# Optimization experiments

Measured on AMD Instinct MI355X. Metric: run time of the kernel, lower is better.

The kernel has to match this reference:

```python
import jax, jax.numpy as jnp
import numpy as np

K = 7          # kernel_size
PAD = 3        # padding
GROUPS = 8
OUTC = 128
INC = 128
REFINE = True


def conv1x1(x, w):
    # x: [B,C,H,W], w: [O,C] (1x1 conv, no bias)
    return jnp.einsum('oc,bchw->bohw', w, x)


def unfold2d(x, k):
    # x: [B,C,Hp,Wp] -> [B,C,h,w,k,k], stride 1 (matches torch unfold(2,k).unfold(3,k))
    B, C, Hp, Wp = x.shape
    h, w = Hp - k + 1, Wp - k + 1
    patches = jnp.stack([x[:, :, i:i + h, j:j + w] for i in range(k) for j in range(k)], axis=-1)
    return patches.reshape(B, C, h, w, k, k)


def unfold1d(x, k, axis):
    # sliding window of size k, stride 1, along axis 2 (rows) or 3 (cols)
    if axis == 2:
        h = x.shape[2] - k + 1
        return jnp.stack([x[:, :, i:i + h, :] for i in range(k)], axis=-1)  # [B,C,h,W,k]
    else:
        w = x.shape[3] - k + 1
        return jnp.stack([x[:, :, :, j:j + w] for j in range(k)], axis=-1)  # [B,C,H,w,k]


def _forward(feature_map, wq, wk, wv, rel_h, rel_w):
    c = feature_map.shape[1] // 2
    fm_t0, fm_t1 = feature_map[:, :c], feature_map[:, c:]
    B, _, H, W = fm_t0.shape
    cg = OUTC // GROUPS

    padded_t0 = jnp.pad(fm_t0, ((0, 0), (0, 0), (PAD, PAD), (PAD, PAD)))
    q = conv1x1(fm_t1, wq)                 # [B,OUTC,H,W]
    k_full = conv1x1(padded_t0, wk)        # [B,OUTC,H+2p,W+2p]
    v_full = conv1x1(padded_t0, wv)

    k_win = unfold2d(k_full, K)            # [B,OUTC,H,W,K,K]
    k_h, k_w = k_win[:, :OUTC // 2], k_win[:, OUTC // 2:]
    k_win = jnp.concatenate([k_h + rel_h, k_w + rel_w], axis=1)
    k_win = k_win.reshape(B, GROUPS, cg, H, W, K * K)
    v_win = unfold2d(v_full, K).reshape(B, GROUPS, cg, H, W, K * K)

    qg = q.reshape(B, GROUPS, cg, H, W, 1)
    attn = jax.nn.softmax(jnp.sum(qg * k_win, axis=2), axis=-1)  # [B,G,H,W,K*K]
    out = jnp.einsum('bnhwk,bnchwk->bnchw', attn, v_win).reshape(B, OUTC, H, W)

    if REFINE:
        win = 2 * K + 1
        p_col = jnp.pad(fm_t0, ((0, 0), (0, 0), (K, K), (0, 0)))
        p_row = jnp.pad(fm_t0, ((0, 0), (0, 0), (0, 0), (K, K)))
        k_col = unfold1d(conv1x1(p_col, wk), win, 2).reshape(B, GROUPS, cg, H, W, win)
        k_row = unfold1d(conv1x1(p_row, wk), win, 3).reshape(B, GROUPS, cg, H, W, win)
        v_col = unfold1d(conv1x1(p_col, wv), win, 2).reshape(B, GROUPS, cg, H, W, win)
        v_row = unfold1d(conv1x1(p_row, wv), win, 3).reshape(B, GROUPS, cg, H, W, win)

        a_row = jax.nn.softmax(jnp.sum(qg * k_row, axis=2), axis=-1)
        a_col = jax.nn.softmax(jnp.sum(qg * k_col, axis=2), axis=-1)
        out = out + jnp.einsum('bnhwk,bnchwk->bnchw', a_row, v_row).reshape(B, OUTC, H, W)
        out = out + jnp.einsum('bnhwk,bnchwk->bnchw', a_col, v_col).reshape(B, OUTC, H, W)
    return out


def setup_inputs() -> dict:
    key = jax.random.key(0)
    ks = jax.random.split(key, 6)
    B, H, W = 2, 64, 64
    feature_map = jax.random.normal(ks[0], (B, 2 * INC, H, W), dtype=jnp.float32)
    # kaiming_normal fan_out for 1x1 conv: std = sqrt(2 / outc)
    std = float(np.sqrt(2.0 / OUTC))
    wq = jax.random.normal(ks[1], (OUTC, INC), dtype=jnp.float32) * std
    wk = jax.random.normal(ks[2], (OUTC, INC), dtype=jnp.float32) * std
    wv = jax.random.normal(ks[3], (OUTC, INC), dtype=jnp.float32) * std
    rel_h = jax.random.normal(ks[4], (OUTC // 2, 1, 1, K, 1), dtype=jnp.float32)
    rel_w = jax.random.normal(ks[5], (OUTC // 2, 1, 1, 1, K), dtype=jnp.float32)
    return {"feature_map": feature_map, "wq": wq, "wk": wk, "wv": wv,
            "rel_h": rel_h, "rel_w": rel_w}


def reference(feature_map, wq, wk, wv, rel_h, rel_w):
    return _forward(feature_map, wq, wk, wv, rel_h, rel_w)
```

## Files before the change

kernel.cpp:

```cpp
#include <hip/hip_runtime.h>
#include <hip/hip_bf16.h>

__device__ __forceinline__ float bf2f(unsigned short u) {
    union { unsigned int i; float f; } v; v.i = ((unsigned int)u) << 16; return v.f;
}
__device__ __forceinline__ unsigned short f2bf(float f) {
    __hip_bfloat16 h = __float2bfloat16(f);
    return *reinterpret_cast<unsigned short*>(&h);
}


#define CANVAS_SLAB 102400

__global__ __launch_bounds__(256) void pad_zero_kernel(uint4* __restrict__ p)
{
    const size_t i = (size_t)blockIdx.x * 256 + threadIdx.x;
    p[i] = make_uint4(0u, 0u, 0u, 0u);
}

__global__ __launch_bounds__(256) void conv_kernel(
    const float* __restrict__ fm,
    const float* __restrict__ wq, const float* __restrict__ wk,
    const float* __restrict__ wv,
    float* __restrict__ Qout,
    unsigned short* __restrict__ K0,
    unsigned short* __restrict__ V0)
{
    const int sel = blockIdx.z;
    const int by  = blockIdx.y;
    const float* W = (sel == 0) ? wq : ((sel == 1) ? wk : wv);
    const int c0 = (sel == 0) ? 128 : 0;

    __shared__ float w_s[64 * 68];
    __shared__ float x_s[64 * 68];

    const int tid = threadIdx.x;
    const int P0  = blockIdx.x * 64;
    const int b   = P0 >> 12;
    const int hw0 = P0 & 4095;

    float acc[4][4];
    #pragma unroll
    for (int i = 0; i < 4; ++i)
        #pragma unroll
        for (int j = 0; j < 4; ++j) acc[i][j] = 0.f;

    const int ocb = (tid >> 4) * 4;
    const int pxb = (tid & 15) * 4;

    for (int kh = 0; kh < 128; kh += 64) {
        {
            const int o    = tid >> 2;
            const int koff = (tid & 3) * 16;
            #pragma unroll
            for (int i = 0; i < 4; ++i) {
                float4 v = *(const float4*)(W + (size_t)(by * 64 + o) * 128 + kh + koff + i * 4);
                w_s[(koff + i * 4 + 0) * 68 + o] = v.x;
                w_s[(koff + i * 4 + 1) * 68 + o] = v.y;
                w_s[(koff + i * 4 + 2) * 68 + o] = v.z;
                w_s[(koff + i * 4 + 3) * 68 + o] = v.w;
            }
        }
        {
            const int c  = tid >> 2;
            const int pc = (tid & 3) * 16;
            const float* src = fm + (((size_t)(b * 256 + c0 + kh + c)) << 12) + hw0 + pc;
            #pragma unroll
            for (int i = 0; i < 4; ++i)
                *(float4*)(&x_s[c * 68 + pc + i * 4]) = *(const float4*)(src + i * 4);
        }
        __syncthreads();
        #pragma unroll 8
        for (int k = 0; k < 64; ++k) {
            float4 wa = *(const float4*)(&w_s[k * 68 + ocb]);
            float4 xv = *(const float4*)(&x_s[k * 68 + pxb]);
            const float wf[4] = {wa.x, wa.y, wa.z, wa.w};
            const float xf[4] = {xv.x, xv.y, xv.z, xv.w};
            #pragma unroll
            for (int i = 0; i < 4; ++i)
                #pragma unroll
                for (int j = 0; j < 4; ++j) acc[i][j] += wf[i] * xf[j];
        }
        __syncthreads();
    }

    const int oc  = by * 64 + ocb;
    const int g   = oc >> 4;
    const int lci = oc & 15;
    const int hh  = hw0 >> 6;
    #pragma unroll
    for (int pj = 0; pj < 4; ++pj) {
        const int ww = pxb + pj;
        if (sel == 0) {
            const size_t base = ((((size_t)(b * 8 + g)) << 12) + (hh * 64 + ww)) * 16 + lci;
            *(float4*)(Qout + base) = make_float4(acc[0][pj], acc[1][pj], acc[2][pj], acc[3][pj]);
        } else {
            const size_t cbase = (size_t)(b * 8 + g) * CANVAS_SLAB
                               + ((size_t)((hh + 8) * 80 + (ww + 8))) * 16 + lci;
            unsigned short tmp[4];
            #pragma unroll
            for (int i = 0; i < 4; ++i) tmp[i] = f2bf(acc[i][pj]);
            unsigned short* dst = ((sel == 1) ? K0 : V0) + cbase;
            *(uint2*)dst = *(const uint2*)tmp;
        }
    }
}

struct KV16 { uint4 a, b; };
__device__ __forceinline__ KV16 ld16(const unsigned short* p) {
    KV16 r; r.a = *(const uint4*)p; r.b = *(const uint4*)(p + 8); return r;
}
__device__ __forceinline__ float dotq(const float* q, const KV16& k) {
    const unsigned short* u = (const unsigned short*)&k;
    float s = 0.f;
    #pragma unroll
    for (int c = 0; c < 16; ++c) s += q[c] * bf2f(u[c]);
    return s;
}
__device__ __forceinline__ void axpyq(float* acc, float wgt, const KV16& v) {
    const unsigned short* u = (const unsigned short*)&v;
    #pragma unroll
    for (int c = 0; c < 16; ++c) acc[c] += wgt * bf2f(u[c]);
}

__global__ __launch_bounds__(256) void attn_kernel(
    const float* __restrict__ Q,
    const unsigned short* __restrict__ K0,
    const unsigned short* __restrict__ V0,
    const float* __restrict__ rel_h,
    const float* __restrict__ rel_w,
    float* __restrict__ out)
{
    const int tid  = threadIdx.x;
    const int w    = tid & 63;
    const int h    = blockIdx.x * 4 + (tid >> 6);
    const int g    = blockIdx.y;
    const int b    = blockIdx.z / 3;
    const int part = blockIdx.z % 3;

    const size_t slabQ = ((size_t)(b * 8 + g)) << 16;
    const float* qptr = Q + slabQ + (size_t)(h * 64 + w) * 16;

    float qr[16];
    #pragma unroll
    for (int ci = 0; ci < 16; ++ci) qr[ci] = qptr[ci];

    const unsigned short* Kp = K0 + (size_t)(b * 8 + g) * CANVAS_SLAB;
    const unsigned short* Vp = V0 + (size_t)(b * 8 + g) * CANVAS_SLAB;

    #define CIDX(y, x) (((size_t)(((y) + 8) * 80 + ((x) + 8))) << 4)

    float acc[16];
    #pragma unroll
    for (int ci = 0; ci < 16; ++ci) acc[ci] = 0.f;

    if (part == 0) {
        float qrel[7];
        const float* rel = (g < 4) ? (rel_h + g * 112) : (rel_w + (g - 4) * 112);
        #pragma unroll
        for (int t = 0; t < 7; ++t) {
            float s = 0.f;
            #pragma unroll
            for (int ci = 0; ci < 16; ++ci) s += qr[ci] * rel[ci * 7 + t];
            qrel[t] = s;
        }
        const bool bias_i = (g < 4);
        float sc[49];
        float mx = -3.4e38f;
        #pragma unroll
        for (int i = 0; i < 7; ++i) {
            const int y = h + i - 3;
            #pragma unroll
            for (int j = 0; j < 7; ++j) {
                const int x = w + j - 3;
                float d = dotq(qr, ld16(Kp + CIDX(y, x)));
                d += bias_i ? qrel[i] : qrel[j];
                sc[i * 7 + j] = d;
                mx = fmaxf(mx, d);
            }
        }
        float den = 0.f;
        #pragma unroll
        for (int k = 0; k < 49; ++k) { sc[k] = __expf(sc[k] - mx); den += sc[k]; }
        const float inv = 1.f / den;
        #pragma unroll
        for (int i = 0; i < 7; ++i) {
            const int y = h + i - 3;
            #pragma unroll
            for (int j = 0; j < 7; ++j) {
                const int x = w + j - 3;
                axpyq(acc, sc[i * 7 + j] * inv, ld16(Vp + CIDX(y, x)));
            }
        }
    } else if (part == 1) {
        float sc[15];
        float mx = -3.4e38f;
        #pragma unroll
        for (int j = 0; j < 15; ++j) {
            const int x = w + j - 7;
            const float d = dotq(qr, ld16(Kp + CIDX(h, x)));
            sc[j] = d; mx = fmaxf(mx, d);
        }
        float den = 0.f;
        #pragma unroll
        for (int j = 0; j < 15; ++j) { sc[j] = __expf(sc[j] - mx); den += sc[j]; }
        const float inv = 1.f / den;
        #pragma unroll
        for (int j = 0; j < 15; ++j) {
            const int x = w + j - 7;
            axpyq(acc, sc[j] * inv, ld16(Vp + CIDX(h, x)));
        }
    } else {
        float sc[15];
        float mx = -3.4e38f;
        #pragma unroll
        for (int i = 0; i < 15; ++i) {
            const int y = h + i - 7;
            const float d = dotq(qr, ld16(Kp + CIDX(y, w)));
            sc[i] = d; mx = fmaxf(mx, d);
        }
        float den = 0.f;
        #pragma unroll
        for (int i = 0; i < 15; ++i) { sc[i] = __expf(sc[i] - mx); den += sc[i]; }
        const float inv = 1.f / den;
        #pragma unroll
        for (int i = 0; i < 15; ++i) {
            const int y = h + i - 7;
            axpyq(acc, sc[i] * inv, ld16(Vp + CIDX(y, w)));
        }
    }
    #undef CIDX

    float* op = out + (((size_t)(b * 128 + g * 16)) << 12) + h * 64 + w;
    #pragma unroll
    for (int ci = 0; ci < 16; ++ci)
        atomicAdd(op + ((size_t)ci << 12), acc[ci]);
}

extern "C" void kernel_launch(void* const* d_in, const int* in_sizes, int n_in,
                              void* d_out, int out_size, void* d_ws, size_t ws_size,
                              hipStream_t stream) {
    (void)in_sizes; (void)n_in; (void)ws_size;
    const float* fm    = (const float*)d_in[0];
    const float* wq    = (const float*)d_in[1];
    const float* wk    = (const float*)d_in[2];
    const float* wv    = (const float*)d_in[3];
    const float* rel_h = (const float*)d_in[4];
    const float* rel_w = (const float*)d_in[5];

    float* Q = (float*)d_ws;
    unsigned short* K0 = (unsigned short*)(Q + 1048576);
    unsigned short* V0 = K0 + 16 * CANVAS_SLAB;

    hipMemsetAsync(d_out, 0, (size_t)out_size * sizeof(float), stream);
    pad_zero_kernel<<<dim3(1600), dim3(256), 0, stream>>>((uint4*)K0);

    conv_kernel<<<dim3(128, 2, 3), dim3(256), 0, stream>>>(
        fm, wq, wk, wv, Q, K0, V0);
    attn_kernel<<<dim3(16, 8, 6), dim3(256), 0, stream>>>(
        Q, K0, V0, rel_h, rel_w, (float*)d_out);
}
```

Baseline: 111.5 us.

## Stage K/V halo rows into swizzled shared memory for attention windows

The attention kernel now cooperatively copies the K rows covering each block's window halo into an XOR-swizzled LDS buffer, computes scores from LDS, then restages V into the same buffer for the weighted sum. This replaces many redundant global/L2 loads of overlapping neighbourhoods with reads from shared memory. The cost is extra barriers, a serialized stage/compute pattern with no overlap, and up to 46KB of LDS per block, which may reduce occupancy.

```diff
diff --git a/kernel.cpp b/kernel.cpp
--- a/kernel.cpp
+++ b/kernel.cpp
@@ -107,9 +107,6 @@
 }
 
 struct KV16 { uint4 a, b; };
-__device__ __forceinline__ KV16 ld16(const unsigned short* p) {
-    KV16 r; r.a = *(const uint4*)p; r.b = *(const uint4*)(p + 8); return r;
-}
 __device__ __forceinline__ float dotq(const float* q, const KV16& k) {
     const unsigned short* u = (const unsigned short*)&k;
     float s = 0.f;
@@ -121,6 +118,29 @@
     const unsigned short* u = (const unsigned short*)&v;
     #pragma unroll
     for (int c = 0; c < 16; ++c) acc[c] += wgt * bf2f(u[c]);
+}
+
+__device__ __forceinline__ void stage_rows(unsigned short* kvs,
+    const unsigned short* __restrict__ slab, int R0, int NR, int tid)
+{
+    const int nchunk = NR * 160;
+    for (int c = tid; c < nchunk; c += 256) {
+        const int row  = c / 160;
+        const int rem  = c - row * 160;
+        const int px   = rem >> 1;
+        const int half = rem & 1;
+        const uint4 v = *(const uint4*)(slab + ((size_t)(R0 + row) * 80 + px) * 16 + half * 8);
+        const int dst = row * 1280 + px * 16 + ((half ^ ((px >> 2) & 1)) << 3);
+        *(uint4*)(kvs + dst) = v;
+    }
+}
+__device__ __forceinline__ KV16 lds16(const unsigned short* kvs, int rowIdx, int px) {
+    const int base = rowIdx * 1280 + px * 16;
+    const int sw   = ((px >> 2) & 1) << 3;
+    KV16 r;
+    r.a = *(const uint4*)(kvs + base + sw);
+    r.b = *(const uint4*)(kvs + base + (8 - sw));
+    return r;
 }
 
 __global__ __launch_bounds__(256) void attn_kernel(
@@ -133,28 +153,31 @@
 {
     const int tid  = threadIdx.x;
     const int w    = tid & 63;
-    const int h    = blockIdx.x * 4 + (tid >> 6);
+    const int hr   = tid >> 6;
+    const int h0   = blockIdx.x * 4;
+    const int h    = h0 + hr;
     const int g    = blockIdx.y;
     const int b    = blockIdx.z / 3;
     const int part = blockIdx.z % 3;
 
+    __shared__ __align__(16) unsigned short kvs[18 * 1280];
+
     const size_t slabQ = ((size_t)(b * 8 + g)) << 16;
     const float* qptr = Q + slabQ + (size_t)(h * 64 + w) * 16;
 
-    float qr[16];
-    #pragma unroll
-    for (int ci = 0; ci < 16; ++ci) qr[ci] = qptr[ci];
-
     const unsigned short* Kp = K0 + (size_t)(b * 8 + g) * CANVAS_SLAB;
     const unsigned short* Vp = V0 + (size_t)(b * 8 + g) * CANVAS_SLAB;
 
-    #define CIDX(y, x) (((size_t)(((y) + 8) * 80 + ((x) + 8))) << 4)
+    float qr[16];
+    #pragma unroll
+    for (int ci = 0; ci < 16; ++ci) qr[ci] = qptr[ci];
 
     float acc[16];
     #pragma unroll
     for (int ci = 0; ci < 16; ++ci) acc[ci] = 0.f;
 
     if (part == 0) {
+        stage_rows(kvs, Kp, h0 + 5, 10, tid);
         float qrel[7];
         const float* rel = (g < 4) ? (rel_h + g * 112) : (rel_w + (g - 4) * 112);
         #pragma unroll
@@ -165,15 +188,16 @@
             qrel[t] = s;
         }
         const bool bias_i = (g < 4);
+        __syncthreads();
+
         float sc[49];
         float mx = -3.4e38f;
         #pragma unroll
         for (int i = 0; i < 7; ++i) {
-            const int y = h + i - 3;
+            const int ri = hr + i;
             #pragma unroll
             for (int j = 0; j < 7; ++j) {
-                const int x = w + j - 3;
-                float d = dotq(qr, ld16(Kp + CIDX(y, x)));
+                float d = dotq(qr, lds16(kvs, ri, w + j + 5));
                 d += bias_i ? qrel[i] : qrel[j];
                 sc[i * 7 + j] = d;
                 mx = fmaxf(mx, d);
@@ -183,53 +207,65 @@
         #pragma unroll
         for (int k = 0; k < 49; ++k) { sc[k] = __expf(sc[k] - mx); den += sc[k]; }
         const float inv = 1.f / den;
+
+        __syncthreads();
+        stage_rows(kvs, Vp, h0 + 5, 10, tid);
+        __syncthreads();
+
         #pragma unroll
         for (int i = 0; i < 7; ++i) {
-            const int y = h + i - 3;
-            #pragma unroll
-            for (int j = 0; j < 7; ++j) {
-                const int x = w + j - 3;
-                axpyq(acc, sc[i * 7 + j] * inv, ld16(Vp + CIDX(y, x)));
-            }
+            const int ri = hr + i;
+            #pragma unroll
+            for (int j = 0; j < 7; ++j)
+                axpyq(acc, sc[i * 7 + j] * inv, lds16(kvs, ri, w + j + 5));
         }
     } else if (part == 1) {
+        stage_rows(kvs, Kp, h0 + 8, 4, tid);
+        __syncthreads();
+
         float sc[15];
         float mx = -3.4e38f;
         #pragma unroll
         for (int j = 0; j < 15; ++j) {
-            const int x = w + j - 7;
-            const float d = dotq(qr, ld16(Kp + CIDX(h, x)));
+            const float d = dotq(qr, lds16(kvs, hr, w + j + 1));
             sc[j] = d; mx = fmaxf(mx, d);
         }
         float den = 0.f;
         #pragma unroll
         for (int j = 0; j < 15; ++j) { sc[j] = __expf(sc[j] - mx); den += sc[j]; }
         const float inv = 1.f / den;
-        #pragma unroll
-        for (int j = 0; j < 15; ++j) {
-            const int x = w + j - 7;
-            axpyq(acc, sc[j] * inv, ld16(Vp + CIDX(h, x)));
-        }
+
+        __syncthreads();
+        stage_rows(kvs, Vp, h0 + 8, 4, tid);
+        __syncthreads();
+
+        #pragma unroll
+        for (int j = 0; j < 15; ++j)
+            axpyq(acc, sc[j] * inv, lds16(kvs, hr, w + j + 1));
     } else {
+        stage_rows(kvs, Kp, h0 + 1, 18, tid);
+        __syncthreads();
+
         float sc[15];
         float mx = -3.4e38f;
         #pragma unroll
         for (int i = 0; i < 15; ++i) {
-            const int y = h + i - 7;
-            const float d = dotq(qr, ld16(Kp + CIDX(y, w)));
+            const float d = dotq(qr, lds16(kvs, hr + i, w + 8));
             sc[i] = d; mx = fmaxf(mx, d);
         }
         float den = 0.f;
         #pragma unroll
         for (int i = 0; i < 15; ++i) { sc[i] = __expf(sc[i] - mx); den += sc[i]; }
         const float inv = 1.f / den;
-        #pragma unroll
-        for (int i = 0; i < 15; ++i) {
-            const int y = h + i - 7;
-            axpyq(acc, sc[i] * inv, ld16(Vp + CIDX(y, w)));
-        }
-    }
-    #undef CIDX
+
+        __syncthreads();
+        stage_rows(kvs, Vp, h0 + 1, 18, tid);
+        __syncthreads();
+
+        #pragma unroll
+        for (int i = 0; i < 15; ++i)
+            axpyq(acc, sc[i] * inv, lds16(kvs, hr + i, w + 8));
+    }
 
     float* op = out + (((size_t)(b * 128 + g * 16)) << 12) + h * 64 + w;
     #pragma unroll
```

New measurement: 120.6 us. +8.1%, slower.
